# Optimization experiments

Measured on AMD Instinct MI355X. Metric: run time of the kernel, lower is better.

The kernel has to match this reference:

```python
import jax, jax.numpy as jnp
import numpy as np

N, E, IN, H, T = 100000, 1600000, 10, 64, 10


def setup_inputs() -> dict:
    key = jax.random.key(0)
    ks = jax.random.split(key, 24)
    w = lambda k, shape, s=0.05: jax.random.normal(k, shape, jnp.float32) * s
    return {
        "x": w(ks[0], (N, IN), 1.0),
        "edge_attr": w(ks[1], (E, T), 1.0),
        "gcn1_w": w(ks[2], (IN, H)), "gcn1_b": jnp.zeros((H,), jnp.float32),
        "e_w1": w(ks[3], (3 * T, H)), "e_b1": jnp.zeros((H,), jnp.float32),
        "e_w2": w(ks[4], (H, H)), "e_b2": jnp.zeros((H,), jnp.float32),
        "gcn2_w": w(ks[5], (2 * H, H)), "gcn2_b": jnp.zeros((H,), jnp.float32),
        "gcn3_w": w(ks[6], (H, IN)), "gcn3_b": jnp.zeros((IN,), jnp.float32),
        "l1_w": w(ks[7], (2 * IN, IN)), "l1_b": jnp.zeros((IN,), jnp.float32),
        "l2_w": w(ks[8], (IN, 128)), "l2_b": jnp.zeros((128,), jnp.float32),
        "l3_w": w(ks[9], (128, 32)), "l3_b": jnp.zeros((32,), jnp.float32),
        "l4_w": w(ks[10], (32, 2)), "l4_b": jnp.zeros((2,), jnp.float32),
        "edge_index": jax.random.randint(ks[11], (2, E), 0, N),
    }


def reference(x, edge_attr, gcn1_w, gcn1_b, e_w1, e_b1, e_w2, e_b2,
              gcn2_w, gcn2_b, gcn3_w, gcn3_b, l1_w, l1_b, l2_w, l2_b,
              l3_w, l3_b, l4_w, l4_b, edge_index):
    src, dst = edge_index[0], edge_index[1]  # j -> i (message flows src->dst)
    # GCN symmetric norm with self loops: deg counted on target, +1 self loop
    deg = 1.0 + jax.ops.segment_sum(jnp.ones((E,), jnp.float32), dst, num_segments=N)
    dis = deg ** -0.5  # [N]
    edge_norm = (dis[src] * dis[dst])[:, None]  # [E,1]

    def gcn(h, w, b):
        hw = h @ w  # [N,out]
        agg = jax.ops.segment_sum(hw[src] * edge_norm, dst, num_segments=N)
        agg = agg + hw * (dis * dis)[:, None]  # self-loop term, norm = 1/deg
        return agg + b

    out1 = jax.nn.relu(gcn(x, gcn1_w, gcn1_b))
    # EdgeConv: gather x_i (dst), x_j (src), concat edge_attr, MLP, scatter-max
    m = jnp.concatenate([x[dst], x[src], edge_attr], axis=1)  # [E, 3T]
    m = jax.nn.relu(m @ e_w1 + e_b1) @ e_w2 + e_b2  # [E, H]
    agg = jax.ops.segment_max(m, dst, num_segments=N)
    agg = jnp.where(jnp.isfinite(agg), agg, 0.0)  # isolated nodes -> 0
    oute = jax.nn.relu(agg)

    out2 = jax.nn.relu(gcn(jnp.concatenate([out1, oute], axis=1), gcn2_w, gcn2_b))
    out3 = jax.nn.relu(gcn(out2, gcn3_w, gcn3_b))
    h = jnp.concatenate([x, out3], axis=1)  # [N, 2*IN]
    h = jax.nn.softplus(h @ l1_w + l1_b)
    h = jax.nn.softplus(h @ l2_w + l2_b)
    h = jax.nn.softplus(h @ l3_w + l3_b)
    h = h @ l4_w + l4_b  # [N, 2]
    return (h[:, 0], h[:, 1])
```

## Files before the change

### kernel.cpp

```cpp
#include <hip/hip_runtime.h>
#include <hip/hip_bf16.h>

typedef unsigned int u32;
typedef unsigned short u16;
typedef _Float16 f16;
typedef _Float16 f16x8 __attribute__((ext_vector_type(8)));
typedef float f32x4 __attribute__((ext_vector_type(4)));
typedef u32 u32x4 __attribute__((ext_vector_type(4)));

#define DEV static __device__ __forceinline__

#define O_G1   0
#define O_G1b  640
#define O_W1   704
#define O_B1   2624
#define O_W2   2688
#define O_B2   6784
#define O_G2   6848
#define O_G2b  15040
#define O_G3   15104
#define O_G3b  15744
#define O_L1   15754
#define O_L1b  15954
#define O_L2t  15964
#define O_L2b  17244
#define O_L3   17372
#define O_L3b  21468
#define O_L4t  21500
#define O_L4b  21564
#define O_WF1  21568
#define O_WF2  22592
#define WTOT   24640

#define ECNB   32

DEV float bfu(u16 h){ return __uint_as_float(((u32)h) << 16); }
DEV float bflo(u32 u){ return __uint_as_float(u << 16); }
DEV float bfhi(u32 u){ return __uint_as_float(u & 0xffff0000u); }
DEV u16 f2bf(float x){
  __hip_bfloat16 b = __float2bfloat16(x);
  return *(u16*)&b;
}
DEV float rdf(const void* p, int idx, int isf32){
  return isf32 ? ((const float*)p)[idx] : bfu(((const u16*)p)[idx]);
}
DEV void load10_bf(const u32* __restrict__ p, float* f){
  u32 a0=p[0],a1=p[1],a2=p[2],a3=p[3],a4=p[4];
  f[0]=bflo(a0); f[1]=bfhi(a0);
  f[2]=bflo(a1); f[3]=bfhi(a1);
  f[4]=bflo(a2); f[5]=bfhi(a2);
  f[6]=bflo(a3); f[7]=bfhi(a3);
  f[8]=bflo(a4); f[9]=bfhi(a4);
}
DEV void load10_any(const void* base, size_t row, int isf32, float* f){
  if (isf32){
    const float* p = (const float*)base + row*10;
    #pragma unroll
    for (int k=0;k<10;k++) f[k] = p[k];
  } else {
    load10_bf((const u32*)base + row*5, f);
  }
}
DEV float softplusf(float x){ return fmaxf(x,0.f) + __logf(1.f + __expf(-fabsf(x))); }

DEV int permk(int k){
  if (k < 8)  return k;
  if (k < 16) return 10 + (k-8);
  if (k < 24) return 20 + (k-16);
  if (k == 24) return 8;
  if (k == 25) return 9;
  if (k == 26) return 18;
  if (k == 27) return 19;
  if (k == 28) return 28;
  if (k == 29) return 29;
  return -1;
}
DEV u32 packh2(float a, float b){
  union { f16 h[2]; u32 u; } t;
  t.h[0] = (f16)a; t.h[1] = (f16)b;
  return t.u;
}

__global__ __launch_bounds__(256) void k_detect(
    const u32* p0, const u32* p1, const u32* p2, const u32* p3,
    const u32* p4, const u32* p5, const u32* p6, const u32* p7,
    const u32* p8, const u32* p9, const u32* p10,const u32* p11,
    const u32* p12,const u32* p13,const u32* p14,const u32* p15,
    const u32* p16,const u32* p17,const u32* p18,const u32* p19,
    int* __restrict__ flags, int N_, int E_)
{
  int a = blockIdx.x;
  const u32* p;
  int elems;
  switch (a){
    case 0:  p=p0;  elems=N_*10; break;
    case 1:  p=p1;  elems=E_*10; break;
    case 2:  p=p2;  elems=640;  break;
    case 3:  p=p3;  elems=64;   break;
    case 4:  p=p4;  elems=1920; break;
    case 5:  p=p5;  elems=64;   break;
    case 6:  p=p6;  elems=4096; break;
    case 7:  p=p7;  elems=64;   break;
    case 8:  p=p8;  elems=8192; break;
    case 9:  p=p9;  elems=64;   break;
    case 10: p=p10; elems=640;  break;
    case 11: p=p11; elems=10;   break;
    case 12: p=p12; elems=200;  break;
    case 13: p=p13; elems=10;   break;
    case 14: p=p14; elems=1280; break;
    case 15: p=p15; elems=128;  break;
    case 16: p=p16; elems=4096; break;
    case 17: p=p17; elems=32;   break;
    case 18: p=p18; elems=64;   break;
    default: p=p19; elems=2;    break;
  }
  int nw = elems/2; if (nw > 512) nw = 512; if (nw < 1) nw = 1;
  int localA = 0, localZ = 0;
  for (int i=threadIdx.x; i<nw; i+=256){
    u32 w = p[i];
    u32 ex = (w >> 7) & 0xffu;
    if (ex >= 0x90u) localA++;
    if ((w & 0xffffu) == 0u) localZ++;
  }
  int packed = (localA << 16) | localZ;
  __shared__ int red[4];
  #pragma unroll
  for (int off=32; off; off>>=1) packed += __shfl_down(packed, off);
  if ((threadIdx.x & 63) == 0) red[threadIdx.x>>6] = packed;
  __syncthreads();
  if (threadIdx.x == 0){
    int s = red[0]+red[1]+red[2]+red[3];
    int sA = s >> 16, sZ = s & 0xffff;
    flags[a] = (sA * 16 >= nw || sZ * 4 >= nw * 3) ? 1 : 0;
  }
}

__global__ __launch_bounds__(256) void k_prep(
    const void* g1w, const void* g1b, const void* ew1, const void* eb1,
    const void* ew2, const void* eb2, const void* g2w, const void* g2b,
    const void* g3w, const void* g3b, const void* l1w, const void* l1b,
    const void* l2w, const void* l2b, const void* l3w, const void* l3b,
    const void* l4w, const void* l4b,
    const int* __restrict__ flags, float* __restrict__ W)
{
  int t = threadIdx.x;
  int f2=flags[2],f3=flags[3],f4=flags[4],f5=flags[5],f6=flags[6],f7=flags[7];
  int f8=flags[8],f9=flags[9],f10=flags[10],f11=flags[11],f12=flags[12],f13=flags[13];
  int f14=flags[14],f15=flags[15],f16=flags[16],f17=flags[17],f18=flags[18],f19=flags[19];
  for (int i=t;i<640;i+=256)  W[O_G1+i]  = rdf(g1w,i,f2);
  for (int i=t;i<64;i+=256)   W[O_G1b+i] = rdf(g1b,i,f3);
  for (int i=t;i<1920;i+=256) W[O_W1+i]  = rdf(ew1,i,f4);
  for (int i=t;i<64;i+=256)   W[O_B1+i]  = rdf(eb1,i,f5);
  for (int i=t;i<4096;i+=256) W[O_W2+i]  = rdf(ew2,i,f6);
  for (int i=t;i<64;i+=256)   W[O_B2+i]  = rdf(eb2,i,f7);
  for (int i=t;i<8192;i+=256) W[O_G2+i]  = rdf(g2w,i,f8);
  for (int i=t;i<64;i+=256)   W[O_G2b+i] = rdf(g2b,i,f9);
  for (int i=t;i<640;i+=256)  W[O_G3+i]  = rdf(g3w,i,f10);
  for (int i=t;i<10;i+=256)   W[O_G3b+i] = rdf(g3b,i,f11);
  for (int i=t;i<200;i+=256)  W[O_L1+i]  = rdf(l1w,i,f12);
  for (int i=t;i<10;i+=256)   W[O_L1b+i] = rdf(l1b,i,f13);
  for (int i=t;i<1280;i+=256){ int o=i/10,k=i-o*10; W[O_L2t+i]=rdf(l2w,k*128+o,f14); }
  for (int i=t;i<128;i+=256)  W[O_L2b+i] = rdf(l2b,i,f15);
  for (int i=t;i<4096;i+=256) W[O_L3+i]  = rdf(l3w,i,f16);
  for (int i=t;i<32;i+=256)   W[O_L3b+i] = rdf(l3b,i,f17);
  for (int i=t;i<64;i+=256){ int c=i>>5,j=i&31; W[O_L4t+i]=rdf(l4w,j*2+c,f18); }
  for (int i=t;i<2;i+=256)    W[O_L4b+i] = rdf(l4b,i,f19);
  u32* Wu = (u32*)W;
  for (int i=t;i<1024;i+=256){
    int l=i&63, q=(i>>6)&3, c=i>>8;
    int k0=(l>>4)*8+2*q, col=c*16+(l&15);
    int r0=permk(k0), r1=permk(k0+1);
    float v0 = (r0<0)?0.f:rdf(ew1,r0*64+col,f4);
    float v1 = (r1<0)?0.f:rdf(ew1,r1*64+col,f4);
    Wu[O_WF1+i] = packh2(v0,v1);
  }
  for (int i=t;i<2048;i+=256){
    int l=i&63, q=(i>>6)&3, h2=(i>>8)&1, c=i>>9;
    int k0=32*h2+(l>>4)*8+2*q, col=c*16+(l&15);
    Wu[O_WF2+i] = packh2(rdf(ew2,k0*64+col,f6), rdf(ew2,(k0+1)*64+col,f6));
  }
}

__global__ __launch_bounds__(256) void k_init(int* __restrict__ cnt, int N_)
{
  int i = blockIdx.x*256 + threadIdx.x;
  if (i < N_) cnt[i] = 0;
}

__global__ __launch_bounds__(256) void k_count(const int* __restrict__ ei, int* __restrict__ cnt, int E_)
{
  int e = blockIdx.x*256 + threadIdx.x;
  if (e >= E_) return;
  atomicAdd(&cnt[ei[E_+e]], 1);
}

__global__ __launch_bounds__(1024) void k_bsum(const int* __restrict__ cnt, int* __restrict__ bsum, int N_)
{
  int i = blockIdx.x*1024 + threadIdx.x;
  int v = (i < N_) ? cnt[i] : 0;
  #pragma unroll
  for (int off=32; off; off>>=1) v += __shfl_down(v, off);
  __shared__ int ws_[16];
  if ((threadIdx.x & 63) == 0) ws_[threadIdx.x>>6] = v;
  __syncthreads();
  if (threadIdx.x == 0){
    int s = 0;
    #pragma unroll
    for (int j=0;j<16;j++) s += ws_[j];
    bsum[blockIdx.x] = s;
  }
}

__global__ __launch_bounds__(128) void k_scan_small(const int* __restrict__ bsum, int* __restrict__ boff, int NB)
{
  int t = threadIdx.x;
  int v = (t < NB) ? bsum[t] : 0;
  int lane = t & 63, w = t >> 6;
  int x = v;
  #pragma unroll
  for (int off=1; off<64; off<<=1){ int y=__shfl_up(x,off); if (lane>=off) x+=y; }
  __shared__ int t2[2];
  if (lane==63) t2[w]=x;
  __syncthreads();
  if (w==1) x += t2[0];
  boff[t] = x - v;
}

__global__ __launch_bounds__(1024) void k_scan_final(
    int* __restrict__ cnt, const int* __restrict__ boff,
    int* __restrict__ rp, float* __restrict__ dis, int N_, int E_)
{
  int i = blockIdx.x*1024 + threadIdx.x;
  int v = (i < N_) ? cnt[i] : 0;
  int lane = threadIdx.x & 63, w = threadIdx.x >> 6;
  int x = v;
  #pragma unroll
  for (int off=1; off<64; off<<=1){ int y=__shfl_up(x,off); if (lane>=off) x+=y; }
  __shared__ int wp[16];
  if (lane==63) wp[w]=x;
  __syncthreads();
  if (threadIdx.x==0){
    int run=0;
    #pragma unroll
    for (int j=0;j<16;j++){ int t=wp[j]; wp[j]=run; run+=t; }
  }
  __syncthreads();
  int incl = x + wp[w] + boff[blockIdx.x];
  if (i < N_){
    rp[i]  = incl - v;
    dis[i] = rsqrtf(1.f + (float)v);
    cnt[i] = 0;
  }
  if (i == 0) rp[N_] = E_;
}

__global__ __launch_bounds__(256) void k_fill(
    const int* __restrict__ ei, const int* __restrict__ rp, int* __restrict__ cnt,
    int4* __restrict__ csr, int E_)
{
  int e = blockIdx.x*256 + threadIdx.x;
  if (e >= E_) return;
  int s = ei[e], d = ei[E_+e];
  int pos = rp[d] + atomicAdd(&cnt[d], 1);
  csr[pos] = make_int4(s, e, d, 0);
}

#define EC_EMIT \
  if (run >= 0){ int bb = run*64 + x; \
    atomicMax(&nodemax[bb],    __float_as_int(e0)); \
    atomicMax(&nodemax[bb+16], __float_as_int(e1)); \
    atomicMax(&nodemax[bb+32], __float_as_int(e2)); \
    atomicMax(&nodemax[bb+48], __float_as_int(e3)); }
#define EC_STEP(DD, RR) { \
  float t0=fmaxf(mcv[0][RR],0.f), t1=fmaxf(mcv[1][RR],0.f), \
        t2=fmaxf(mcv[2][RR],0.f), t3=fmaxf(mcv[3][RR],0.f); \
  if (DD == run){ e0=fmaxf(e0,t0); e1=fmaxf(e1,t1); e2=fmaxf(e2,t2); e3=fmaxf(e3,t3); } \
  else { EC_EMIT; run = DD; e0=t0; e1=t1; e2=t2; e3=t3; } }

__global__ __launch_bounds__(256) void k_edgeconv(
    const void* __restrict__ xv, const void* __restrict__ eav,
    const int* __restrict__ rp, const int4* __restrict__ csr,
    const float* __restrict__ W, const int* __restrict__ flags,
    float* __restrict__ oute, int N_, int E_)
{
  __shared__ int nodemax[ECNB*64];
  __shared__ u32 hbuf[4][16*36];
  int tid = threadIdx.x;
  int l = tid & 63, wv = tid >> 6;
  int x = l & 15, g = l >> 4;
  int n0 = blockIdx.x * ECNB;
  if (n0 >= N_) return;
  int nend = n0 + ECNB; if (nend > N_) nend = N_;
  #pragma unroll
  for (int i=0;i<ECNB/4;i++) nodemax[i*256 + tid] = 0;
  int fx = flags[0], fea = flags[1];
  const u32* Wu = (const u32*)W;
  union FU { u32 u[4]; f16x8 v; };
  union HU { f16 h[8]; u32 u[4]; f16x8 v; };
  FU w1u[4];
  #pragma unroll
  for (int c=0;c<4;c++){
    #pragma unroll
    for (int q=0;q<4;q++) w1u[c].u[q] = Wu[O_WF1 + (c*4+q)*64 + l];
  }
  FU w2u[4][2];
  #pragma unroll
  for (int c=0;c<4;c++){
    #pragma unroll
    for (int h=0;h<2;h++){
      #pragma unroll
      for (int q=0;q<4;q++) w2u[c][h].u[q] = Wu[O_WF2 + ((c*2+h)*4+q)*64 + l];
    }
  }
  float b1v[4], b2v[4];
  #pragma unroll
  for (int c=0;c<4;c++){ b1v[c] = (W+O_B1)[c*16 + x]; b2v[c] = (W+O_B2)[c*16 + x]; }
  int pbase = rp[n0], pend = rp[nend];
  int ntiles = (pend - pbase + 15) >> 4;
  u32* hb = hbuf[wv];
  __syncthreads();

  for (int t = wv; t < ntiles; t += 4){
    int p0 = pbase + t*16;
    int eA = p0 + x; if (eA > E_-1) eA = E_-1;
    int4 ce = csr[eA];
    HU af;
    u32 exv = 0;
    if (g < 3){
      long row; const void* base; int isf;
      if (g==0){ row = ce.z; base = xv;  isf = fx; }
      else if (g==1){ row = ce.x; base = xv;  isf = fx; }
      else { row = ce.y; base = eav; isf = fea; }
      if (isf){
        const float* p = (const float*)base + row*10;
        #pragma unroll
        for (int j=0;j<8;j++) af.h[j] = (f16)p[j];
        exv = packh2(p[8], p[9]);
      } else {
        const u32* p = (const u32*)base + row*5;
        u32 a0=p[0],a1=p[1],a2=p[2],a3=p[3],a4=p[4];
        af.h[0]=(f16)bflo(a0); af.h[1]=(f16)bfhi(a0);
        af.h[2]=(f16)bflo(a1); af.h[3]=(f16)bfhi(a1);
        af.h[4]=(f16)bflo(a2); af.h[5]=(f16)bfhi(a2);
        af.h[6]=(f16)bflo(a3); af.h[7]=(f16)bfhi(a3);
        exv = packh2(bflo(a4), bfhi(a4));
      }
    }
    u32 ge0 = (u32)__shfl((int)exv, x);
    u32 ge1 = (u32)__shfl((int)exv, x+16);
    u32 ge2 = (u32)__shfl((int)exv, x+32);
    if (g == 3){ af.u[0]=ge0; af.u[1]=ge1; af.u[2]=ge2; af.u[3]=0; }
    int pe = p0 + 4*g;
    int dz = ce.z;
    int d0 = __shfl(dz, 4*g+0); d0 = (pe   < pend) ? d0 - n0 : -1;
    int d1 = __shfl(dz, 4*g+1); d1 = (pe+1 < pend) ? d1 - n0 : -1;
    int d2 = __shfl(dz, 4*g+2); d2 = (pe+2 < pend) ? d2 - n0 : -1;
    int d3 = __shfl(dz, 4*g+3); d3 = (pe+3 < pend) ? d3 - n0 : -1;
    f32x4 z = {0.f,0.f,0.f,0.f};
    f32x4 hc[4];
    #pragma unroll
    for (int c=0;c<4;c++)
      hc[c] = __builtin_amdgcn_mfma_f32_16x16x32_f16(af.v, w1u[c].v, z, 0, 0, 0);
    #pragma unroll
    for (int r=0;r<4;r++){
      u32 pk0,pk1,pk2,pk3;
      {
        float hv = fmaxf(hc[0][r] + b1v[0], 0.f);
        union { f16 h; u16 u; } cv; cv.h=(f16)hv; u32 mine=cv.u;
        u32 other=(u32)__shfl_xor((int)mine,1,64);
        pk0 = (x&1) ? (other|(mine<<16)) : (mine|(other<<16));
      }{
        float hv = fmaxf(hc[1][r] + b1v[1], 0.f);
        union { f16 h; u16 u; } cv; cv.h=(f16)hv; u32 mine=cv.u;
        u32 other=(u32)__shfl_xor((int)mine,1,64);
        pk1 = (x&1) ? (other|(mine<<16)) : (mine|(other<<16));
      }{
        float hv = fmaxf(hc[2][r] + b1v[2], 0.f);
        union { f16 h; u16 u; } cv; cv.h=(f16)hv; u32 mine=cv.u;
        u32 other=(u32)__shfl_xor((int)mine,1,64);
        pk2 = (x&1) ? (other|(mine<<16)) : (mine|(other<<16));
      }{
        float hv = fmaxf(hc[3][r] + b1v[3], 0.f);
        union { f16 h; u16 u; } cv; cv.h=(f16)hv; u32 mine=cv.u;
        u32 other=(u32)__shfl_xor((int)mine,1,64);
        pk3 = (x&1) ? (other|(mine<<16)) : (mine|(other<<16));
      }
      int edge = 4*g + r;
      int par = (x&1) ? 16 : 0;
      hb[edge*36 + par + (x>>1)]     = (x&1) ? pk2 : pk0;
      hb[edge*36 + 8 + par + (x>>1)] = (x&1) ? pk3 : pk1;
    }
    asm volatile("s_waitcnt lgkmcnt(0)" ::: "memory");
    HU a2f[2];
    #pragma unroll
    for (int h=0;h<2;h++){
      const u32x4* p = (const u32x4*)&hb[x*36 + g*4 + 16*h];
      u32x4 tv = *p;
      a2f[h].u[0]=tv[0]; a2f[h].u[1]=tv[1]; a2f[h].u[2]=tv[2]; a2f[h].u[3]=tv[3];
    }
    f32x4 mcv[4];
    #pragma unroll
    for (int c=0;c<4;c++){
      f32x4 bi = {b2v[c],b2v[c],b2v[c],b2v[c]};
      f32x4 acc = __builtin_amdgcn_mfma_f32_16x16x32_f16(a2f[0].v, w2u[c][0].v, bi, 0, 0, 0);
      mcv[c]    = __builtin_amdgcn_mfma_f32_16x16x32_f16(a2f[1].v, w2u[c][1].v, acc, 0, 0, 0);
    }
    int run = -2; float e0=0.f,e1=0.f,e2=0.f,e3=0.f;
    EC_STEP(d0,0) EC_STEP(d1,1) EC_STEP(d2,2) EC_STEP(d3,3)
    EC_EMIT;
  }
  __syncthreads();
  int tot = (nend - n0) * 64;
  for (int i = tid; i < tot; i += 256)
    oute[(size_t)n0*64 + i] = __int_as_float(nodemax[i]);
}

__global__ __launch_bounds__(256) void k_aggx(
    const void* __restrict__ xv, const int* __restrict__ rp,
    const int4* __restrict__ csr, const float* __restrict__ dis,
    const int* __restrict__ flags, float* __restrict__ sx, int N_)
{
  int i = blockIdx.x*256 + threadIdx.x;
  if (i >= N_) return;
  int fx = flags[0];
  float di = dis[i], d2 = di*di;
  float acc[10], ac2[10], tA[10], tB[10], tC[10], tD[10];
  load10_any(xv, (size_t)i, fx, tA);
  #pragma unroll
  for (int f=0;f<10;f++){ acc[f] = tA[f]*d2; ac2[f] = 0.f; }
  int b = rp[i], en = rp[i+1];
  int p = b;
  for (; p+3 < en; p += 4){
    int s0 = csr[p].x, s1 = csr[p+1].x, s2 = csr[p+2].x, s3 = csr[p+3].x;
    float m0 = dis[s0]*di, m1 = dis[s1]*di, m2 = dis[s2]*di, m3 = dis[s3]*di;
    load10_any(xv, (size_t)s0, fx, tA);
    load10_any(xv, (size_t)s1, fx, tB);
    load10_any(xv, (size_t)s2, fx, tC);
    load10_any(xv, (size_t)s3, fx, tD);
    #pragma unroll
    for (int f=0;f<10;f++){
      acc[f] = fmaf(tA[f], m0, acc[f]);
      ac2[f] = fmaf(tB[f], m1, ac2[f]);
      acc[f] = fmaf(tC[f], m2, acc[f]);
      ac2[f] = fmaf(tD[f], m3, ac2[f]);
    }
  }
  for (; p < en; p++){
    int s0 = csr[p].x; float m0 = dis[s0]*di;
    load10_any(xv, (size_t)s0, fx, tA);
    #pragma unroll
    for (int f=0;f<10;f++) acc[f] = fmaf(tA[f], m0, acc[f]);
  }
  float* o = sx + (size_t)i*10;
  #pragma unroll
  for (int f=0;f<10;f++) o[f] = acc[f] + ac2[f];
}

__global__ __launch_bounds__(256) void k_hw2(
    const float* __restrict__ sx, const float* __restrict__ oute,
    const float* __restrict__ W, u16* __restrict__ hw2o, int N_)
{
  int i = blockIdx.x*256 + threadIdx.x;
  if (i >= N_) return;
  float sv[10];
  const float* srow = sx + (size_t)i*10;
  #pragma unroll
  for (int f=0;f<10;f++) sv[f] = srow[f];
  const float* __restrict__ G1  = W + O_G1;
  const float* __restrict__ G1b = W + O_G1b;
  const float* __restrict__ G2  = W + O_G2;
  float hw[64];
  #pragma unroll
  for (int f=0;f<64;f++) hw[f] = 0.f;
  #pragma unroll 1
  for (int k=0;k<64;k++){
    float o1 = G1b[k];
    #pragma unroll
    for (int j=0;j<10;j++) o1 = fmaf(sv[j], G1[j*64+k], o1);
    o1 = fmaxf(o1, 0.f);
    const float* __restrict__ wt = G2 + k*64;
    #pragma unroll
    for (int f=0;f<64;f++) hw[f] = fmaf(o1, wt[f], hw[f]);
  }
  const float* orow = oute + (size_t)i*64;
  #pragma unroll 1
  for (int k=0;k<64;k++){
    float ov = orow[k];
    const float* __restrict__ wb = G2 + (64+k)*64;
    #pragma unroll
    for (int f=0;f<64;f++) hw[f] = fmaf(ov, wb[f], hw[f]);
  }
  u16* out = hw2o + (size_t)i*64;
  #pragma unroll
  for (int f=0;f<64;f++) out[f] = f2bf(hw[f]);
}

__global__ __launch_bounds__(256) void k_agg64(
    const u16* __restrict__ hw2, const int* __restrict__ rp,
    const int4* __restrict__ csr, const float* __restrict__ dis,
    const float* __restrict__ W, float* __restrict__ out2, int N_)
{
  int i = (blockIdx.x*256 + threadIdx.x) >> 6;
  int lane = threadIdx.x & 63;
  if (i >= N_) return;
  int e4 = lane >> 4, c4 = lane & 15;
  float di = dis[i];
  int b = rp[i], en = rp[i+1];
  const uint2* __restrict__ h2 = (const uint2*)hw2;
  float a0=0.f,a1=0.f,a2=0.f,a3=0.f;
  float b0=0.f,b1=0.f,b2=0.f,b3=0.f;
  int p = b + e4;
  int sA = (p   < en) ? csr[p].x   : 0;
  int sB = (p+4 < en) ? csr[p+4].x : 0;
  for (; p + 4 < en; p += 8){
    int sAn = (p+8  < en) ? csr[p+8].x  : 0;
    int sBn = (p+12 < en) ? csr[p+12].x : 0;
    float nmA = dis[sA]*di, nmB = dis[sB]*di;
    uint2 wA = h2[(size_t)sA*16 + c4];
    uint2 wB = h2[(size_t)sB*16 + c4];
    a0 = fmaf(bflo(wA.x), nmA, a0); a1 = fmaf(bfhi(wA.x), nmA, a1);
    a2 = fmaf(bflo(wA.y), nmA, a2); a3 = fmaf(bfhi(wA.y), nmA, a3);
    b0 = fmaf(bflo(wB.x), nmB, b0); b1 = fmaf(bfhi(wB.x), nmB, b1);
    b2 = fmaf(bflo(wB.y), nmB, b2); b3 = fmaf(bfhi(wB.y), nmB, b3);
    sA = sAn; sB = sBn;
  }
  if (p < en){
    float nmA = dis[sA]*di;
    uint2 wA = h2[(size_t)sA*16 + c4];
    a0 = fmaf(bflo(wA.x), nmA, a0); a1 = fmaf(bfhi(wA.x), nmA, a1);
    a2 = fmaf(bflo(wA.y), nmA, a2); a3 = fmaf(bfhi(wA.y), nmA, a3);
  }
  a0 += b0; a1 += b1; a2 += b2; a3 += b3;
  a0 += __shfl_xor(a0,16); a1 += __shfl_xor(a1,16);
  a2 += __shfl_xor(a2,16); a3 += __shfl_xor(a3,16);
  a0 += __shfl_xor(a0,32); a1 += __shfl_xor(a1,32);
  a2 += __shfl_xor(a2,32); a3 += __shfl_xor(a3,32);
  if (e4 == 0){
    uint2 ws2 = h2[(size_t)i*16 + c4];
    float d2 = di*di;
    const float* G2b = W + O_G2b;
    float4 o;
    o.x = fmaxf(fmaf(bflo(ws2.x), d2, a0) + G2b[4*c4],   0.f);
    o.y = fmaxf(fmaf(bfhi(ws2.x), d2, a1) + G2b[4*c4+1], 0.f);
    o.z = fmaxf(fmaf(bflo(ws2.y), d2, a2) + G2b[4*c4+2], 0.f);
    o.w = fmaxf(fmaf(bfhi(ws2.y), d2, a3) + G2b[4*c4+3], 0.f);
    *(float4*)(out2 + (size_t)i*64 + 4*c4) = o;
  }
}

__global__ __launch_bounds__(256) void k_hw3(
    const float* __restrict__ out2, const float* __restrict__ W,
    float* __restrict__ hw3, int N_)
{
  int i = blockIdx.x*256 + threadIdx.x;
  if (i >= N_) return;
  const float* row = out2 + (size_t)i*64;
  const float* __restrict__ G3 = W + O_G3;
  float a[10];
  #pragma unroll
  for (int f=0;f<10;f++) a[f] = 0.f;
  #pragma unroll 1
  for (int k=0;k<64;k++){
    float v = row[k];
    const float* __restrict__ w = G3 + k*10;
    #pragma unroll
    for (int f=0;f<10;f++) a[f] = fmaf(v, w[f], a[f]);
  }
  float* o = hw3 + (size_t)i*10;
  #pragma unroll
  for (int f=0;f<10;f++) o[f] = a[f];
}

__global__ __launch_bounds__(256) void k_final(
    const void* __restrict__ xv, const float* __restrict__ hw3,
    const int* __restrict__ rp, const int4* __restrict__ csr,
    const float* __restrict__ dis, const int* __restrict__ flags,
    const float* __restrict__ W, float* __restrict__ out, int N_)
{
  int i = blockIdx.x*256 + threadIdx.x;
  if (i >= N_) return;
  int fx = flags[0];
  float di = dis[i];
  float a[10], a2v[10];
  const float* hrow = hw3 + (size_t)i*10;
  #pragma unroll
  for (int f=0;f<10;f++){ a[f] = hrow[f]*di*di; a2v[f] = 0.f; }
  int b = rp[i], en = rp[i+1];
  int p = b;
  for (; p+3 < en; p += 4){
    int s0 = csr[p].x, s1 = csr[p+1].x, s2 = csr[p+2].x, s3 = csr[p+3].x;
    float m0 = dis[s0]*di, m1 = dis[s1]*di, m2 = dis[s2]*di, m3 = dis[s3]*di;
    const float* r0p = hw3 + (size_t)s0*10;
    const float* r1p = hw3 + (size_t)s1*10;
    const float* r2p = hw3 + (size_t)s2*10;
    const float* r3p = hw3 + (size_t)s3*10;
    #pragma unroll
    for (int f=0;f<10;f++){
      a[f]   = fmaf(r0p[f], m0, a[f]);
      a2v[f] = fmaf(r1p[f], m1, a2v[f]);
      a[f]   = fmaf(r2p[f], m2, a[f]);
      a2v[f] = fmaf(r3p[f], m3, a2v[f]);
    }
  }
  for (; p < en; p++){
    int s0 = csr[p].x; float m0 = dis[s0]*di;
    const float* r0p = hw3 + (size_t)s0*10;
    #pragma unroll
    for (int f=0;f<10;f++) a[f] = fmaf(r0p[f], m0, a[f]);
  }
  #pragma unroll
  for (int f=0;f<10;f++) a[f] += a2v[f];
  const float* G3b = W + O_G3b;
  float h20[20];
  load10_any(xv, (size_t)i, fx, h20);
  #pragma unroll
  for (int f=0;f<10;f++) h20[10+f] = fmaxf(a[f] + G3b[f], 0.f);
  const float* __restrict__ L1  = W + O_L1;
  const float* __restrict__ L1b = W + O_L1b;
  float h1[10];
  #pragma unroll
  for (int f=0;f<10;f++) h1[f] = L1b[f];
  #pragma unroll
  for (int k=0;k<20;k++){
    float v = h20[k];
    const float* __restrict__ w = L1 + k*10;
    #pragma unroll
    for (int f=0;f<10;f++) h1[f] = fmaf(v, w[f], h1[f]);
  }
  #pragma unroll
  for (int f=0;f<10;f++) h1[f] = softplusf(h1[f]);
  const float* __restrict__ L2t = W + O_L2t;
  const float* __restrict__ L2b = W + O_L2b;
  const float* __restrict__ L3  = W + O_L3;
  const float* __restrict__ L3b = W + O_L3b;
  float h3a[32], h3b[32];
  #pragma unroll
  for (int j=0;j<32;j++){ h3a[j] = L3b[j]; h3b[j] = 0.f; }
  #pragma unroll 1
  for (int o=0;o<64;o++){
    float sA = L2b[o], sB = L2b[o+64];
    const float* __restrict__ wtA = L2t + o*10;
    const float* __restrict__ wtB = L2t + (o+64)*10;
    #pragma unroll
    for (int k=0;k<10;k++){
      sA = fmaf(h1[k], wtA[k], sA);
      sB = fmaf(h1[k], wtB[k], sB);
    }
    sA = softplusf(sA);
    sB = softplusf(sB);
    const float* __restrict__ w3A = L3 + o*32;
    const float* __restrict__ w3B = L3 + (o+64)*32;
    #pragma unroll
    for (int j=0;j<32;j++){
      h3a[j] = fmaf(sA, w3A[j], h3a[j]);
      h3b[j] = fmaf(sB, w3B[j], h3b[j]);
    }
  }
  const float* L4t = W + O_L4t;
  const float* L4b = W + O_L4b;
  float r0 = L4b[0], r1 = L4b[1];
  #pragma unroll
  for (int j=0;j<32;j++){
    float h3 = softplusf(h3a[j] + h3b[j]);
    r0 = fmaf(h3, L4t[j],    r0);
    r1 = fmaf(h3, L4t[32+j], r1);
  }
  out[i]      = r0;
  out[N_ + i] = r1;
}

extern "C" void kernel_launch(void* const* d_in, const int* in_sizes, int n_in,
                              void* d_out, int out_size, void* d_ws, size_t ws_size,
                              hipStream_t stream)
{
  const void* xv  = d_in[0];
  const void* eav = d_in[1];
  const int*  ei  = (const int*)d_in[20];
  int N_ = in_sizes[0] / 10;
  int E_ = in_sizes[1] / 10;

  float* W = (float*)d_ws;
  size_t off = WTOT;
  int*   cnt   = (int*)(W + off);   off += (size_t)N_;
  int*   rp    = (int*)(W + off);   off += (size_t)N_ + 1;
  float* dis   = (float*)(W + off); off += (size_t)N_;
  int*   bsum  = (int*)(W + off);   off += 256;
  int*   boff  = (int*)(W + off);   off += 256;
  int*   flags = (int*)(W + off);   off += 32;
  off = (off + 3) & ~(size_t)3;
  int4*  csr   = (int4*)(W + off);  off += (size_t)E_ * 4;
  float* oute  = (float*)(W + off);
  float* out2  = oute;
  off += (size_t)N_ * 64;
  u16*   hw2   = (u16*)(W + off);   off += (size_t)N_ * 32;
  float* sx    = (float*)(W + off);
  float* hw3   = sx;
  off += (size_t)N_ * 10;

  if (ws_size < off * sizeof(float)) return;

  int gN = (N_ + 255)/256, gE = (E_ + 255)/256;
  int NB = (N_ + 1023)/1024;

  k_detect<<<20,256,0,stream>>>(
      (const u32*)d_in[0],(const u32*)d_in[1],
      (const u32*)d_in[2],(const u32*)d_in[3],(const u32*)d_in[4],(const u32*)d_in[5],
      (const u32*)d_in[6],(const u32*)d_in[7],(const u32*)d_in[8],(const u32*)d_in[9],
      (const u32*)d_in[10],(const u32*)d_in[11],(const u32*)d_in[12],(const u32*)d_in[13],
      (const u32*)d_in[14],(const u32*)d_in[15],(const u32*)d_in[16],(const u32*)d_in[17],
      (const u32*)d_in[18],(const u32*)d_in[19],
      flags, N_, E_);
  k_prep<<<1,256,0,stream>>>(
      d_in[2],d_in[3],d_in[4],d_in[5],d_in[6],d_in[7],d_in[8],d_in[9],
      d_in[10],d_in[11],d_in[12],d_in[13],d_in[14],d_in[15],d_in[16],d_in[17],
      d_in[18],d_in[19], flags, W);
  k_init<<<gN,256,0,stream>>>(cnt, N_);
  k_count<<<gE,256,0,stream>>>(ei, cnt, E_);
  k_bsum<<<NB,1024,0,stream>>>(cnt, bsum, N_);
  k_scan_small<<<1,128,0,stream>>>(bsum, boff, NB);
  k_scan_final<<<NB,1024,0,stream>>>(cnt, boff, rp, dis, N_, E_);
  k_fill<<<gE,256,0,stream>>>(ei, rp, cnt, csr, E_);
  k_edgeconv<<<(N_+ECNB-1)/ECNB,256,0,stream>>>(xv, eav, rp, csr, W, flags, oute, N_, E_);
  k_aggx<<<gN,256,0,stream>>>(xv, rp, csr, dis, flags, sx, N_);
  k_hw2<<<gN,256,0,stream>>>(sx, oute, W, hw2, N_);
  k_agg64<<<(N_+3)/4,256,0,stream>>>(hw2, rp, csr, dis, W, out2, N_);
  k_hw3<<<gN,256,0,stream>>>(out2, W, hw3, N_);
  k_final<<<gN,256,0,stream>>>(xv, hw3, rp, csr, dis, flags, W,
                               (float*)d_out, N_);
}
```

Before: 680.1 us.

## Record per-edge rank in count pass; build CSR via inverse permutation

The count kernel now saves the atomicAdd return value as each edge's rank within its destination, so the fill pass no longer needs a second round of atomics. CSR construction is split into two passes. The first scatters 4-byte edge ids to their sorted positions. The second walks those positions in order and writes the int4 CSR records with coalesced stores while gathering src and dst. This trades the random 16-byte scatter and contended atomics for an extra kernel launch and extra rank/inv traffic, with rank and inv aliased onto the oute and hw2 buffers when they fit.

```diff
diff --git a/kernel.cpp b/kernel.cpp
--- a/kernel.cpp
+++ b/kernel.cpp
@@ -187,11 +187,13 @@
   if (i < N_) cnt[i] = 0;
 }
 
-__global__ __launch_bounds__(256) void k_count(const int* __restrict__ ei, int* __restrict__ cnt, int E_)
+__global__ __launch_bounds__(256) void k_count(
+    const int* __restrict__ ei, int* __restrict__ cnt,
+    int* __restrict__ rank, int E_)
 {
   int e = blockIdx.x*256 + threadIdx.x;
   if (e >= E_) return;
-  atomicAdd(&cnt[ei[E_+e]], 1);
+  rank[e] = atomicAdd(&cnt[ei[E_+e]], 1);
 }
 
 __global__ __launch_bounds__(1024) void k_bsum(const int* __restrict__ cnt, int* __restrict__ bsum, int N_)
@@ -249,20 +251,28 @@
   if (i < N_){
     rp[i]  = incl - v;
     dis[i] = rsqrtf(1.f + (float)v);
-    cnt[i] = 0;
   }
   if (i == 0) rp[N_] = E_;
 }
 
-__global__ __launch_bounds__(256) void k_fill(
-    const int* __restrict__ ei, const int* __restrict__ rp, int* __restrict__ cnt,
-    int4* __restrict__ csr, int E_)
+__global__ __launch_bounds__(256) void k_fillpos(
+    const int* __restrict__ ei, const int* __restrict__ rank,
+    const int* __restrict__ rp, int* __restrict__ inv, int E_)
 {
   int e = blockIdx.x*256 + threadIdx.x;
   if (e >= E_) return;
-  int s = ei[e], d = ei[E_+e];
-  int pos = rp[d] + atomicAdd(&cnt[d], 1);
-  csr[pos] = make_int4(s, e, d, 0);
+  int d = ei[E_+e];
+  inv[rp[d] + rank[e]] = e;
+}
+
+__global__ __launch_bounds__(256) void k_fillcsr(
+    const int* __restrict__ ei, const int* __restrict__ inv,
+    int4* __restrict__ csr, int E_)
+{
+  int p = blockIdx.x*256 + threadIdx.x;
+  if (p >= E_) return;
+  int e = inv[p];
+  csr[p] = make_int4(ei[e], e, ei[E_+e], 0);
 }
 
 #define EC_EMIT \
@@ -697,6 +707,13 @@
   float* hw3   = sx;
   off += (size_t)N_ * 10;
 
+  int* rank;
+  if ((size_t)E_ <= (size_t)N_ * 64) rank = (int*)oute;
+  else { rank = (int*)(W + off); off += (size_t)E_; }
+  int* inv;
+  if ((size_t)E_ <= (size_t)N_ * 32) inv = (int*)hw2;
+  else { inv = (int*)(W + off); off += (size_t)E_; }
+
   if (ws_size < off * sizeof(float)) return;
 
   int gN = (N_ + 255)/256, gE = (E_ + 255)/256;
@@ -715,11 +732,12 @@
       d_in[10],d_in[11],d_in[12],d_in[13],d_in[14],d_in[15],d_in[16],d_in[17],
       d_in[18],d_in[19], flags, W);
   k_init<<<gN,256,0,stream>>>(cnt, N_);
-  k_count<<<gE,256,0,stream>>>(ei, cnt, E_);
+  k_count<<<gE,256,0,stream>>>(ei, cnt, rank, E_);
   k_bsum<<<NB,1024,0,stream>>>(cnt, bsum, N_);
   k_scan_small<<<1,128,0,stream>>>(bsum, boff, NB);
   k_scan_final<<<NB,1024,0,stream>>>(cnt, boff, rp, dis, N_, E_);
-  k_fill<<<gE,256,0,stream>>>(ei, rp, cnt, csr, E_);
+  k_fillpos<<<gE,256,0,stream>>>(ei, rank, rp, inv, E_);
+  k_fillcsr<<<gE,256,0,stream>>>(ei, inv, csr, E_);
   k_edgeconv<<<(N_+ECNB-1)/ECNB,256,0,stream>>>(xv, eav, rp, csr, W, flags, oute, N_, E_);
   k_aggx<<<gN,256,0,stream>>>(xv, rp, csr, dis, flags, sx, N_);
   k_hw2<<<gN,256,0,stream>>>(sx, oute, W, hw2, N_);
```

New measurement: 645.7 us. -5.1%, faster.
